# Performance work log

Measured on AMD Instinct MI355X. Metric: run time of the kernel, lower is better.

Reference implementation:

```python
import jax, jax.numpy as jnp
import numpy as np

B, S, D_IN, D_OUT, M = 64, 2048, 768, 768, 16


def _lstm_layer(x, Wih, Whh, bih, bhh):
    """PyTorch-convention LSTM layer. x: [B,S,I], Wih: [4H,I], Whh: [4H,H]. Gate order i,f,g,o."""
    H = Whh.shape[1]
    # precompute input contributions for all timesteps (one big GEMM)
    xg = jnp.einsum('bsi,gi->bsg', x, Wih) + bih + bhh  # [B,S,4H]

    def step(carry, xt):
        h, c = carry
        g = xt + h @ Whh.T
        i, f, gg, o = jnp.split(g, 4, axis=-1)
        i = jax.nn.sigmoid(i)
        f = jax.nn.sigmoid(f)
        gg = jnp.tanh(gg)
        o = jax.nn.sigmoid(o)
        c = f * c + i * gg
        h = o * jnp.tanh(c)
        return (h, c), h

    h0 = jnp.zeros((x.shape[0], H), x.dtype)
    _, hs = jax.lax.scan(step, (h0, h0), jnp.swapaxes(xg, 0, 1))
    return jnp.swapaxes(hs, 0, 1)  # [B,S,H]


def setup_inputs() -> dict:
    key = jax.random.key(0)
    ks = jax.random.split(key, 24)
    sc = 0.05
    n = lambda k, shp: jax.random.normal(k, shp, dtype=jnp.float32) * sc
    inp = {
        'x': jax.random.normal(ks[0], (B, S, D_IN), dtype=jnp.float32),
        # manifold_encoder: Linear(D_IN, 2M) -> ReLU -> Linear(2M, M)
        'We1': n(ks[1], (2 * M, D_IN)), 'be1': n(ks[2], (2 * M,)),
        'We2': n(ks[3], (M, 2 * M)), 'be2': n(ks[4], (M,)),
        # 2-layer LSTM(M, M)
        'Wih0': n(ks[5], (4 * M, M)), 'Whh0': n(ks[6], (4 * M, M)),
        'bih0': n(ks[7], (4 * M,)), 'bhh0': n(ks[8], (4 * M,)),
        'Wih1': n(ks[9], (4 * M, M)), 'Whh1': n(ks[10], (4 * M, M)),
        'bih1': n(ks[11], (4 * M,)), 'bhh1': n(ks[12], (4 * M,)),
        # consistency_net: Linear(2M, M) -> ReLU -> Linear(M, 1) -> Sigmoid
        'Wc1': n(ks[13], (M, 2 * M)), 'bc1': n(ks[14], (M,)),
        'Wc2': n(ks[15], (1, M)), 'bc2': n(ks[16], (1,)),
        # manifold_decoder: Linear(M, 2*D_OUT) -> ReLU -> Linear(2*D_OUT, D_OUT)
        'Wd1': n(ks[17], (2 * D_OUT, M)), 'bd1': n(ks[18], (2 * D_OUT,)),
        'Wd2': n(ks[19], (D_OUT, 2 * D_OUT)), 'bd2': n(ks[20], (D_OUT,)),
    }
    return inp


def reference(x, We1, be1, We2, be2, Wih0, Whh0, bih0, bhh0, Wih1, Whh1, bih1, bhh1,
              Wc1, bc1, Wc2, bc2, Wd1, bd1, Wd2, bd2):
    eps = 1e-8
    # manifold encoder
    h = jax.nn.relu(x @ We1.T + be1)
    emb = h @ We2.T + be2  # [B,S,M]

    # flow predictor (2-layer LSTM)
    f0 = _lstm_layer(emb, Wih0, Whh0, bih0, bhh0)
    flow = _lstm_layer(f0, Wih1, Whh1, bih1, bhh1)  # [B,S,M]

    # manifold curvature (vectorized over interior timesteps, zeros at ends)
    prev, curr, nxt = emb[:, :-2], emb[:, 1:-1], emb[:, 2:]
    first = jnp.linalg.norm(curr - prev, axis=-1)
    second = jnp.linalg.norm(nxt - 2.0 * curr + prev, axis=-1)
    curv_int = second / (first + eps)  # [B,S-2]
    zero = jnp.zeros((emb.shape[0], 1), emb.dtype)
    curvature = jnp.concatenate([zero, curv_int, zero], axis=1)  # [B,S]

    # consistency scores between adjacent flow states (vectorized)
    ci = jnp.concatenate([flow[:, :-1], flow[:, 1:]], axis=-1)  # [B,S-1,2M]
    ch = jax.nn.relu(ci @ Wc1.T + bc1)
    cons = jax.nn.sigmoid(ch @ Wc2.T + bc2)[..., 0]  # [B,S-1]
    consistency = jnp.concatenate([cons, cons[:, -1:]], axis=1)  # [B,S]

    curv_w = 1.0 / (curvature + eps)
    weighted = flow * consistency[..., None] * curv_w[..., None]
    temporal = weighted.mean(axis=1)  # [B,M]

    out = jax.nn.relu(temporal @ Wd1.T + bd1) @ Wd2.T + bd2  # [B,D_OUT]
    return out
```

## Files before the change

kernel.cpp:

```cpp
#include <hip/hip_runtime.h>

#define S_LEN 2048
#define BATCH 64

__device__ __forceinline__ float exp2f_fast(float x){ return __builtin_amdgcn_exp2f(x); }
__device__ __forceinline__ float rcpf_fast(float x){ return __builtin_amdgcn_rcpf(x); }
__device__ __forceinline__ float sigmoid_f(float x){
    return rcpf_fast(1.f + exp2f_fast(x * -1.44269504089f));
}
__device__ __forceinline__ float tanh_f(float x){
    return fmaf(rcpf_fast(1.f + exp2f_fast(x * -2.88539008178f)), 2.f, -1.f);
}
__device__ __forceinline__ float readlane_f(float v, int lane){
    return __builtin_bit_cast(float, __builtin_amdgcn_readlane(__builtin_bit_cast(int, v), lane));
}
__device__ __forceinline__ void swap16(float& a, float& b){
    asm("v_permlane16_swap_b32 %0, %1" : "+v"(a), "+v"(b));
}
__device__ __forceinline__ void swap32(float& a, float& b){
    asm("v_permlane32_swap_b32 %0, %1" : "+v"(a), "+v"(b));
}

__global__ __launch_bounds__(256) void k1_embed(
    const float* __restrict__ x, const float* __restrict__ We1, const float* __restrict__ be1,
    const float* __restrict__ We2, const float* __restrict__ be2,
    const float* __restrict__ Wih0, const float* __restrict__ bih0, const float* __restrict__ bhh0,
    float* __restrict__ emb, float* __restrict__ xg0)
{
    __shared__ float tile[2][256*36];
    const int tid = threadIdx.x;
    const size_t row0 = (size_t)blockIdx.x * 256;
    const float* __restrict__ xbase = x + row0 * 768;

    float h1[32];
    #pragma unroll
    for (int o = 0; o < 32; ++o) h1[o] = be1[o];

    float4 st[8];
    #pragma unroll
    for (int it = 0; it < 8; ++it) {
        const int L = it*256 + tid, rr = L >> 3, c4 = L & 7;
        st[it] = *reinterpret_cast<const float4*>(xbase + (size_t)rr*768 + 4*c4);
    }
    #pragma unroll
    for (int it = 0; it < 8; ++it) {
        const int L = it*256 + tid, rr = L >> 3, c4 = L & 7;
        *reinterpret_cast<float4*>(&tile[0][rr*36 + 4*c4]) = st[it];
    }
    __syncthreads();

    for (int c = 0; c < 24; ++c) {
        const int cb = c & 1;
        if (c < 23) {
            const int kc = (c+1)*32;
            #pragma unroll
            for (int it = 0; it < 8; ++it) {
                const int L = it*256 + tid, rr = L >> 3, c4 = L & 7;
                st[it] = *reinterpret_cast<const float4*>(xbase + (size_t)rr*768 + kc + 4*c4);
            }
        }
        float4 xv[8];
        #pragma unroll
        for (int q = 0; q < 8; ++q)
            xv[q] = *reinterpret_cast<const float4*>(&tile[cb][tid*36 + 4*q]);
        const int kc0 = c*32;
        #pragma unroll
        for (int o = 0; o < 32; ++o) {
            const float* wrow = We1 + (size_t)o*768 + kc0;
            float a0=0.f, a1=0.f, a2=0.f, a3=0.f;
            #pragma unroll
            for (int q = 0; q < 8; ++q) {
                float4 wv = *reinterpret_cast<const float4*>(wrow + 4*q);
                a0 = fmaf(xv[q].x, wv.x, a0);
                a1 = fmaf(xv[q].y, wv.y, a1);
                a2 = fmaf(xv[q].z, wv.z, a2);
                a3 = fmaf(xv[q].w, wv.w, a3);
            }
            h1[o] += (a0+a1)+(a2+a3);
        }
        __syncthreads();
        if (c < 23) {
            #pragma unroll
            for (int it = 0; it < 8; ++it) {
                const int L = it*256 + tid, rr = L >> 3, c4 = L & 7;
                *reinterpret_cast<float4*>(&tile[cb^1][rr*36 + 4*c4]) = st[it];
            }
        }
        __syncthreads();
    }

    #pragma unroll
    for (int o = 0; o < 32; ++o) h1[o] = fmaxf(h1[o], 0.f);

    const size_t row = row0 + tid;
    float e2[16];
    #pragma unroll
    for (int m = 0; m < 16; ++m) {
        float acc = be2[m];
        #pragma unroll
        for (int h = 0; h < 32; ++h) acc = fmaf(We2[m*32+h], h1[h], acc);
        e2[m] = acc;
    }
    float4* embo = reinterpret_cast<float4*>(emb + row*16);
    #pragma unroll
    for (int m = 0; m < 4; ++m)
        embo[m] = make_float4(e2[4*m], e2[4*m+1], e2[4*m+2], e2[4*m+3]);

    float* xgo = xg0 + row*64;
    #pragma unroll
    for (int g = 0; g < 16; ++g) {
        float4 v;
        float* vp = &v.x;
        #pragma unroll
        for (int q = 0; q < 4; ++q) {
            const int rr = 4*g + q;
            float acc = bih0[rr] + bhh0[rr];
            #pragma unroll
            for (int m = 0; m < 16; ++m) acc = fmaf(Wih0[rr*16+m], e2[m], acc);
            vp[q] = acc;
        }
        *reinterpret_cast<float4*>(xgo + 4*g) = v;
    }
}

__global__ __launch_bounds__(256) void k1b_curv(const float* __restrict__ emb,
                                                float* __restrict__ curvw)
{
    const int idx = blockIdx.x * 256 + threadIdx.x;
    const int t = idx & (S_LEN-1);
    float cw;
    if (t == 0 || t == S_LEN-1) {
        cw = 1.f / 1e-8f;
    } else {
        const float* e = emb + (size_t)idx * 16;
        float s1 = 0.f, s2 = 0.f;
        #pragma unroll
        for (int m = 0; m < 16; m += 4) {
            float4 p = *(const float4*)(e - 16 + m);
            float4 c = *(const float4*)(e + m);
            float4 n = *(const float4*)(e + 16 + m);
            float d0 = c.x-p.x, d1 = c.y-p.y, d2 = c.z-p.z, d3 = c.w-p.w;
            s1 += d0*d0 + d1*d1 + d2*d2 + d3*d3;
            float e0 = n.x-2.f*c.x+p.x, e1 = n.y-2.f*c.y+p.y;
            float e2_ = n.z-2.f*c.z+p.z, e3 = n.w-2.f*c.w+p.w;
            s2 += e0*e0 + e1*e1 + e2_*e2_ + e3*e3;
        }
        float first = sqrtf(s1), second = sqrtf(s2);
        float curv = second / (first + 1e-8f);
        cw = 1.f / (curv + 1e-8f);
    }
    curvw[idx] = cw;
}

__global__ __launch_bounds__(64) void k2_scan(
    const float* __restrict__ xg0,
    const float* __restrict__ Whh0,
    const float* __restrict__ Wih1, const float* __restrict__ Whh1,
    const float* __restrict__ bih1, const float* __restrict__ bhh1,
    float* __restrict__ flow)
{
    const int r = threadIdx.x;
    const int j = r & 15;
    const int gr = r >> 4;
    const bool grOdd = (gr & 1) != 0;
    const bool grHi  = gr >= 2;
    const bool isg   = (gr == 2);
    const int b = blockIdx.x;
    const float* __restrict__ xgp = xg0 + (size_t)b * S_LEN * 64 + r;

    float wA[16], wI[16], wH[16];
    #pragma unroll
    for (int m = 0; m < 16; ++m) {
        wA[m] = Whh0[r*16+m];
        wI[m] = Wih1[r*16+m];
        wH[m] = Whh1[r*16+m];
    }
    const float biasB = bih1[r] + bhh1[r];
    const float kMul = isg ? -2.88539008178f : -1.44269504089f;
    const float kScl = isg ? 2.f : 1.f;
    const float kOff = isg ? -1.f : 0.f;

    float vAs[16], vBs[16];
    #pragma unroll
    for (int m = 0; m < 16; ++m) { vAs[m] = 0.f; vBs[m] = 0.f; }
    float cA = 0.f, cB = 0.f;

    float xq0 = xgp[0], xq1 = xgp[64], xq2 = xgp[128], xq3 = xgp[192];
    const float* pf = xgp + 256;
    float* stp = flow + (size_t)b * S_LEN * 16 + j;

    auto act = [&](float a) -> float {
        return fmaf(rcpf_fast(1.f + exp2f_fast(a * kMul)), kScl, kOff);
    };
    auto exch = [&](float z, float& gi, float& gf, float& gg, float& go) {
        float za = z, zb = z;  swap16(za, zb);
        float v1 = grOdd ? za : zb;
        float ya = z, yb = z;  swap32(ya, yb);
        float v2 = grHi ? ya : yb;
        float wa = v2, wb = v2; swap16(wa, wb);
        float v3 = grOdd ? wa : wb;
        float A0 = grOdd ? v1 : z;
        float A1 = grOdd ? z  : v1;
        float B0 = grOdd ? v3 : v2;
        float B1 = grOdd ? v2 : v3;
        gi = grHi ? B0 : A0;
        gf = grHi ? B1 : A1;
        gg = grHi ? A0 : B0;
        go = grHi ? A1 : B1;
    };

    auto step = [&](float& xslot, bool doL1) {
        const float xgcur = xslot;
        xslot = *pf; pf += 64;

        float a00 = xgcur, a01 = 0.f, a02 = 0.f, a03 = 0.f;
        #pragma unroll
        for (int m = 0; m < 16; m += 4) {
            a00 = fmaf(vAs[m+0], wA[m+0], a00);
            a01 = fmaf(vAs[m+1], wA[m+1], a01);
            a02 = fmaf(vAs[m+2], wA[m+2], a02);
            a03 = fmaf(vAs[m+3], wA[m+3], a03);
        }
        const float a0 = (a00+a01)+(a02+a03);
        float a10 = biasB, a11 = 0.f, a12 = 0.f, a13 = 0.f;
        #pragma unroll
        for (int m = 0; m < 16; m += 4) {
            a10 = fmaf(vAs[m+0], wI[m+0], a10);
            a11 = fmaf(vAs[m+1], wI[m+1], a11);
            a12 = fmaf(vAs[m+2], wI[m+2], a12);
            a13 = fmaf(vAs[m+3], wI[m+3], a13);
            a10 = fmaf(vBs[m+0], wH[m+0], a10);
            a11 = fmaf(vBs[m+1], wH[m+1], a11);
            a12 = fmaf(vBs[m+2], wH[m+2], a12);
            a13 = fmaf(vBs[m+3], wH[m+3], a13);
        }
        const float a1 = (a10+a11)+(a12+a13);

        float z0 = act(a0);
        float i0, f0, g0, o0;
        exch(z0, i0, f0, g0, o0);
        cA = fmaf(f0, cA, i0*g0);
        const float hA = o0 * tanh_f(cA);
        #pragma unroll
        for (int m = 0; m < 16; ++m) vAs[m] = readlane_f(hA, m);

        if (doL1) {
            float z1 = act(a1);
            float i1, f1, g1, o1;
            exch(z1, i1, f1, g1, o1);
            cB = fmaf(f1, cB, i1*g1);
            const float hB = o1 * tanh_f(cB);
            if (r < 16) *stp = hB;
            stp += 16;
            #pragma unroll
            for (int m = 0; m < 16; ++m) vBs[m] = readlane_f(hB, m);
        }
    };

    step(xq0, false);
    step(xq1, true);
    step(xq2, true);
    step(xq3, true);
    for (int it = 1; it < 512; ++it) {
        step(xq0, true);
        step(xq1, true);
        step(xq2, true);
        step(xq3, true);
    }
    {
        float a10 = biasB, a11 = 0.f, a12 = 0.f, a13 = 0.f;
        #pragma unroll
        for (int m = 0; m < 16; m += 4) {
            a10 = fmaf(vAs[m+0], wI[m+0], a10);
            a11 = fmaf(vAs[m+1], wI[m+1], a11);
            a12 = fmaf(vAs[m+2], wI[m+2], a12);
            a13 = fmaf(vAs[m+3], wI[m+3], a13);
            a10 = fmaf(vBs[m+0], wH[m+0], a10);
            a11 = fmaf(vBs[m+1], wH[m+1], a11);
            a12 = fmaf(vBs[m+2], wH[m+2], a12);
            a13 = fmaf(vBs[m+3], wH[m+3], a13);
        }
        const float a1 = (a10+a11)+(a12+a13);
        float z1 = act(a1);
        float i1, f1, g1, o1;
        exch(z1, i1, f1, g1, o1);
        cB = fmaf(f1, cB, i1*g1);
        const float hB = o1 * tanh_f(cB);
        if (r < 16) *stp = hB;
    }
}

__global__ __launch_bounds__(256) void k3_cons(
    const float* __restrict__ flow, const float* __restrict__ curvw,
    const float* __restrict__ Wc1, const float* __restrict__ bc1,
    const float* __restrict__ Wc2, const float* __restrict__ bc2,
    float* __restrict__ partials)
{
    const int b = blockIdx.x >> 1;
    const int half = blockIdx.x & 1;
    float p[16];
    #pragma unroll
    for (int m = 0; m < 16; ++m) p[m] = 0.f;

    for (int k = 0; k < 4; ++k) {
        const int t = half*1024 + k*256 + threadIdx.x;
        const int c = (t < S_LEN-1) ? t : (S_LEN-2);
        const float* __restrict__ fp = flow + ((size_t)b*S_LEN + c)*16;
        float fa[16], fb[16];
        #pragma unroll
        for (int m = 0; m < 16; m += 4) {
            float4 v = *(const float4*)(fp + m);
            fa[m]=v.x; fa[m+1]=v.y; fa[m+2]=v.z; fa[m+3]=v.w;
            float4 w = *(const float4*)(fp + 16 + m);
            fb[m]=w.x; fb[m+1]=w.y; fb[m+2]=w.z; fb[m+3]=w.w;
        }
        float s = bc2[0];
        #pragma unroll
        for (int h = 0; h < 16; ++h) {
            float ch = bc1[h];
            #pragma unroll
            for (int k2 = 0; k2 < 16; ++k2) ch = fmaf(Wc1[h*32+k2], fa[k2], ch);
            #pragma unroll
            for (int k2 = 0; k2 < 16; ++k2) ch = fmaf(Wc1[h*32+16+k2], fb[k2], ch);
            s = fmaf(Wc2[h], fmaxf(ch, 0.f), s);
        }
        float cons = sigmoid_f(s);
        float w = cons * curvw[(size_t)b*S_LEN + t];
        const bool last = (t == S_LEN-1);
        #pragma unroll
        for (int m = 0; m < 16; ++m) p[m] = fmaf(w, last ? fb[m] : fa[m], p[m]);
    }
    #pragma unroll
    for (int d = 1; d < 64; d <<= 1) {
        #pragma unroll
        for (int m = 0; m < 16; ++m) p[m] += __shfl_xor(p[m], d, 64);
    }
    if ((threadIdx.x & 63) == 0) {
        const int wv = threadIdx.x >> 6;
        float* o = partials + ((size_t)b*8 + half*4 + wv)*16;
        #pragma unroll
        for (int m = 0; m < 16; ++m) o[m] = p[m];
    }
}

__global__ __launch_bounds__(256) void k4_head(
    const float* __restrict__ partials,
    const float* __restrict__ Wd1, const float* __restrict__ bd1,
    const float* __restrict__ Wd2, const float* __restrict__ bd2,
    float* __restrict__ out)
{
    __shared__ __align__(16) float T[16];
    __shared__ __align__(16) float R[1536];
    const int b = blockIdx.x / 3;
    const int ot = blockIdx.x % 3;
    if (threadIdx.x < 16) {
        float s = 0.f;
        #pragma unroll
        for (int cch = 0; cch < 8; ++cch)
            s += partials[((size_t)b*8 + cch)*16 + threadIdx.x];
        T[threadIdx.x] = s * (1.f/2048.f);
    }
    __syncthreads();
    #pragma unroll
    for (int hh = 0; hh < 6; ++hh) {
        int h = hh*256 + threadIdx.x;
        float s = bd1[h];
        #pragma unroll
        for (int m = 0; m < 16; ++m) s = fmaf(Wd1[h*16+m], T[m], s);
        R[h] = fmaxf(s, 0.f);
    }
    __syncthreads();
    const int o = (ot<<8) + threadIdx.x;
    float s = bd2[o];
    const float* wr = Wd2 + (size_t)o*1536;
    for (int h = 0; h < 1536; h += 4) {
        float4 w = *(const float4*)(wr + h);
        float4 rr = *(const float4*)(&R[h]);
        s += w.x*rr.x + w.y*rr.y + w.z*rr.z + w.w*rr.w;
    }
    out[(size_t)b*768 + o] = s;
}

extern "C" void kernel_launch(void* const* d_in, const int* in_sizes, int n_in,
                              void* d_out, int out_size, void* d_ws, size_t ws_size,
                              hipStream_t stream)
{
    const float* x    = (const float*)d_in[0];
    const float* We1  = (const float*)d_in[1];
    const float* be1  = (const float*)d_in[2];
    const float* We2  = (const float*)d_in[3];
    const float* be2  = (const float*)d_in[4];
    const float* Wih0 = (const float*)d_in[5];
    const float* Whh0 = (const float*)d_in[6];
    const float* bih0 = (const float*)d_in[7];
    const float* bhh0 = (const float*)d_in[8];
    const float* Wih1 = (const float*)d_in[9];
    const float* Whh1 = (const float*)d_in[10];
    const float* bih1 = (const float*)d_in[11];
    const float* bhh1 = (const float*)d_in[12];
    const float* Wc1  = (const float*)d_in[13];
    const float* bc1  = (const float*)d_in[14];
    const float* Wc2  = (const float*)d_in[15];
    const float* bc2  = (const float*)d_in[16];
    const float* Wd1  = (const float*)d_in[17];
    const float* bd1  = (const float*)d_in[18];
    const float* Wd2  = (const float*)d_in[19];
    const float* bd2  = (const float*)d_in[20];
    float* out = (float*)d_out;

    float* ws    = (float*)d_ws;
    float* emb   = ws;
    float* xg0   = emb + 2097152;
    float* flow  = xg0 + 8388608;
    float* curvw = flow + 2097152;
    float* parts = curvw + 131072;

    k1_embed<<<dim3(512), dim3(256), 0, stream>>>(x, We1, be1, We2, be2,
                                                  Wih0, bih0, bhh0, emb, xg0);
    k1b_curv<<<dim3(512), dim3(256), 0, stream>>>(emb, curvw);
    k2_scan<<<dim3(64), dim3(64), 0, stream>>>(xg0, Whh0, Wih1, Whh1, bih1, bhh1, flow);
    k3_cons<<<dim3(128), dim3(256), 0, stream>>>(flow, curvw, Wc1, bc1, Wc2, bc2, parts);
    k4_head<<<dim3(192), dim3(256), 0, stream>>>(parts, Wd1, bd1, Wd2, bd2, out);
}
```

Before: 1.140 ms.

## Fuse curvature, consistency and decoder head into one post-scan kernel

Removes the separate curvature kernel and decoder-head kernel. Curvature weights are now recomputed inside the consistency kernel, and the per-batch partial sums are reduced in shared memory before the decoder head runs in the same block. This saves two kernel launches and the global round-trips for curvw and partials. In exchange the tail runs on only 64 blocks of 512 threads instead of 128 plus 192 blocks, so the Wd2 GEMV has less parallelism: each thread handles up to two output rows.

```diff
diff --git a/kernel.cpp b/kernel.cpp
--- a/kernel.cpp
+++ b/kernel.cpp
@@ -121,35 +121,6 @@
         }
         *reinterpret_cast<float4*>(xgo + 4*g) = v;
     }
-}
-
-__global__ __launch_bounds__(256) void k1b_curv(const float* __restrict__ emb,
-                                                float* __restrict__ curvw)
-{
-    const int idx = blockIdx.x * 256 + threadIdx.x;
-    const int t = idx & (S_LEN-1);
-    float cw;
-    if (t == 0 || t == S_LEN-1) {
-        cw = 1.f / 1e-8f;
-    } else {
-        const float* e = emb + (size_t)idx * 16;
-        float s1 = 0.f, s2 = 0.f;
-        #pragma unroll
-        for (int m = 0; m < 16; m += 4) {
-            float4 p = *(const float4*)(e - 16 + m);
-            float4 c = *(const float4*)(e + m);
-            float4 n = *(const float4*)(e + 16 + m);
-            float d0 = c.x-p.x, d1 = c.y-p.y, d2 = c.z-p.z, d3 = c.w-p.w;
-            s1 += d0*d0 + d1*d1 + d2*d2 + d3*d3;
-            float e0 = n.x-2.f*c.x+p.x, e1 = n.y-2.f*c.y+p.y;
-            float e2_ = n.z-2.f*c.z+p.z, e3 = n.w-2.f*c.w+p.w;
-            s2 += e0*e0 + e1*e1 + e2_*e2_ + e3*e3;
-        }
-        float first = sqrtf(s1), second = sqrtf(s2);
-        float curv = second / (first + 1e-8f);
-        cw = 1.f / (curv + 1e-8f);
-    }
-    curvw[idx] = cw;
 }
 
 __global__ __launch_bounds__(64) void k2_scan(
@@ -290,20 +261,28 @@
     }
 }
 
-__global__ __launch_bounds__(256) void k3_cons(
-    const float* __restrict__ flow, const float* __restrict__ curvw,
+__global__ __launch_bounds__(512) void k3_cons_head(
+    const float* __restrict__ emb, const float* __restrict__ flow,
     const float* __restrict__ Wc1, const float* __restrict__ bc1,
     const float* __restrict__ Wc2, const float* __restrict__ bc2,
-    float* __restrict__ partials)
+    const float* __restrict__ Wd1, const float* __restrict__ bd1,
+    const float* __restrict__ Wd2, const float* __restrict__ bd2,
+    float* __restrict__ out)
 {
-    const int b = blockIdx.x >> 1;
-    const int half = blockIdx.x & 1;
+    __shared__ __align__(16) float parts_s[8][16];
+    __shared__ __align__(16) float T[16];
+    __shared__ __align__(16) float R[1536];
+    const int b = blockIdx.x;
+    const int tid = threadIdx.x;
+    const int half = tid >> 8;
+    const int tid256 = tid & 255;
+
     float p[16];
     #pragma unroll
     for (int m = 0; m < 16; ++m) p[m] = 0.f;
 
     for (int k = 0; k < 4; ++k) {
-        const int t = half*1024 + k*256 + threadIdx.x;
+        const int t = half*1024 + k*256 + tid256;
         const int c = (t < S_LEN-1) ? t : (S_LEN-2);
         const float* __restrict__ fp = flow + ((size_t)b*S_LEN + c)*16;
         float fa[16], fb[16];
@@ -325,7 +304,30 @@
             s = fmaf(Wc2[h], fmaxf(ch, 0.f), s);
         }
         float cons = sigmoid_f(s);
-        float w = cons * curvw[(size_t)b*S_LEN + t];
+
+        float cw;
+        if (t == 0 || t == S_LEN-1) {
+            cw = 1.f / 1e-8f;
+        } else {
+            const float* e = emb + ((size_t)b*S_LEN + t) * 16;
+            float s1 = 0.f, s2 = 0.f;
+            #pragma unroll
+            for (int m = 0; m < 16; m += 4) {
+                float4 pp = *(const float4*)(e - 16 + m);
+                float4 cc = *(const float4*)(e + m);
+                float4 nn = *(const float4*)(e + 16 + m);
+                float d0 = cc.x-pp.x, d1 = cc.y-pp.y, d2 = cc.z-pp.z, d3 = cc.w-pp.w;
+                s1 += d0*d0 + d1*d1 + d2*d2 + d3*d3;
+                float e0 = nn.x-2.f*cc.x+pp.x, e1 = nn.y-2.f*cc.y+pp.y;
+                float e2_ = nn.z-2.f*cc.z+pp.z, e3 = nn.w-2.f*cc.w+pp.w;
+                s2 += e0*e0 + e1*e1 + e2_*e2_ + e3*e3;
+            }
+            float first = sqrtf(s1), second = sqrtf(s2);
+            float curv = second / (first + 1e-8f);
+            cw = 1.f / (curv + 1e-8f);
+        }
+
+        float w = cons * cw;
         const bool last = (t == S_LEN-1);
         #pragma unroll
         for (int m = 0; m < 16; ++m) p[m] = fmaf(w, last ? fb[m] : fa[m], p[m]);
@@ -335,50 +337,40 @@
         #pragma unroll
         for (int m = 0; m < 16; ++m) p[m] += __shfl_xor(p[m], d, 64);
     }
-    if ((threadIdx.x & 63) == 0) {
-        const int wv = threadIdx.x >> 6;
-        float* o = partials + ((size_t)b*8 + half*4 + wv)*16;
-        #pragma unroll
-        for (int m = 0; m < 16; ++m) o[m] = p[m];
-    }
-}
-
-__global__ __launch_bounds__(256) void k4_head(
-    const float* __restrict__ partials,
-    const float* __restrict__ Wd1, const float* __restrict__ bd1,
-    const float* __restrict__ Wd2, const float* __restrict__ bd2,
-    float* __restrict__ out)
-{
-    __shared__ __align__(16) float T[16];
-    __shared__ __align__(16) float R[1536];
-    const int b = blockIdx.x / 3;
-    const int ot = blockIdx.x % 3;
-    if (threadIdx.x < 16) {
+    if ((tid & 63) == 0) {
+        const int wv = tid >> 6;
+        #pragma unroll
+        for (int m = 0; m < 16; ++m) parts_s[wv][m] = p[m];
+    }
+    __syncthreads();
+
+    if (tid < 16) {
         float s = 0.f;
         #pragma unroll
         for (int cch = 0; cch < 8; ++cch)
-            s += partials[((size_t)b*8 + cch)*16 + threadIdx.x];
-        T[threadIdx.x] = s * (1.f/2048.f);
+            s += parts_s[cch][tid];
+        T[tid] = s * (1.f/2048.f);
     }
     __syncthreads();
     #pragma unroll
-    for (int hh = 0; hh < 6; ++hh) {
-        int h = hh*256 + threadIdx.x;
+    for (int hh = 0; hh < 3; ++hh) {
+        int h = hh*512 + tid;
         float s = bd1[h];
         #pragma unroll
         for (int m = 0; m < 16; ++m) s = fmaf(Wd1[h*16+m], T[m], s);
         R[h] = fmaxf(s, 0.f);
     }
     __syncthreads();
-    const int o = (ot<<8) + threadIdx.x;
-    float s = bd2[o];
-    const float* wr = Wd2 + (size_t)o*1536;
-    for (int h = 0; h < 1536; h += 4) {
-        float4 w = *(const float4*)(wr + h);
-        float4 rr = *(const float4*)(&R[h]);
-        s += w.x*rr.x + w.y*rr.y + w.z*rr.z + w.w*rr.w;
-    }
-    out[(size_t)b*768 + o] = s;
+    for (int o = tid; o < 768; o += 512) {
+        float s = bd2[o];
+        const float* wr = Wd2 + (size_t)o*1536;
+        for (int h = 0; h < 1536; h += 4) {
+            float4 w = *(const float4*)(wr + h);
+            float4 rr = *(const float4*)(&R[h]);
+            s += w.x*rr.x + w.y*rr.y + w.z*rr.z + w.w*rr.w;
+        }
+        out[(size_t)b*768 + o] = s;
+    }
 }
 
 extern "C" void kernel_launch(void* const* d_in, const int* in_sizes, int n_in,
@@ -412,13 +404,10 @@
     float* emb   = ws;
     float* xg0   = emb + 2097152;
     float* flow  = xg0 + 8388608;
-    float* curvw = flow + 2097152;
-    float* parts = curvw + 131072;
 
     k1_embed<<<dim3(512), dim3(256), 0, stream>>>(x, We1, be1, We2, be2,
                                                   Wih0, bih0, bhh0, emb, xg0);
-    k1b_curv<<<dim3(512), dim3(256), 0, stream>>>(emb, curvw);
     k2_scan<<<dim3(64), dim3(64), 0, stream>>>(xg0, Whh0, Wih1, Whh1, bih1, bhh1, flow);
-    k3_cons<<<dim3(128), dim3(256), 0, stream>>>(flow, curvw, Wc1, bc1, Wc2, bc2, parts);
-    k4_head<<<dim3(192), dim3(256), 0, stream>>>(parts, Wd1, bd1, Wd2, bd2, out);
-}
+    k3_cons_head<<<dim3(64), dim3(512), 0, stream>>>(emb, flow, Wc1, bc1, Wc2, bc2,
+                                                     Wd1, bd1, Wd2, bd2, out);
+}
```

Result: slower. 1.179 ms (+3.4%).
